# Kernel optimization log

Hardware: AMD Instinct MI355X
Metric: run time of the kernel (lower is better)

Reference implementation:

```python
import jax, jax.numpy as jnp
import numpy as np

WS = 7            # window size
NH = 8            # num heads
C = 128           # hidden size
HS = C // NH      # head size = 16


def _rel_index(ws):
    # Swin-style relative position index for a ws x ws window -> [N, N]
    coords = np.stack(np.meshgrid(np.arange(ws), np.arange(ws), indexing='ij'), 0).reshape(2, -1)
    rel = coords[:, :, None] - coords[:, None, :] + (ws - 1)  # [2, N, N] in [0, 2ws-2]
    return jnp.asarray(rel[0] * (2 * ws - 1) + rel[1])        # [N, N] in [0, (2ws-1)^2)


def setup_inputs() -> dict:
    key = jax.random.key(0)
    ks = jax.random.split(key, 6)
    B, H, W = 16, 112, 112
    s = 0.02
    return {
        'x': jax.random.normal(ks[0], (B, H, W, C), jnp.float32),
        'w_q': jax.random.normal(ks[1], (C, C), jnp.float32) * s,
        'w_k': jax.random.normal(ks[2], (C, C), jnp.float32) * s,
        'w_v': jax.random.normal(ks[3], (C, C), jnp.float32) * s,
        'w_o': jax.random.normal(ks[4], (C, C), jnp.float32) * s,
        'b_o': jnp.zeros((C,), jnp.float32),
        'rel_bias': jax.random.normal(ks[5], ((2 * WS - 1) ** 2, NH), jnp.float32) * s,
    }


def reference(x, w_q, w_k, w_v, w_o, b_o, rel_bias):
    B, H, W, Cc = x.shape
    ws = WS
    N = ws * ws
    # window partition: [B,H,W,C] -> [B*nH*nW, ws*ws, C]
    xw = x.reshape(B, H // ws, ws, W // ws, ws, Cc)
    xw = xw.transpose(0, 1, 3, 2, 4, 5).reshape(-1, N, Cc)
    # qkv projections, split heads: [nW, N, C] -> [nW, NH, N, HS]
    scale = HS ** -0.5
    q = (xw @ w_q).reshape(-1, N, NH, HS).transpose(0, 2, 1, 3) * scale
    k = (xw @ w_k).reshape(-1, N, NH, HS).transpose(0, 2, 1, 3)
    v = (xw @ w_v).reshape(-1, N, NH, HS).transpose(0, 2, 1, 3)
    # attention logits + relative position bias
    attn = jnp.einsum('bhnd,bhmd->bhnm', q, k)
    bias = rel_bias[_rel_index(ws)].transpose(2, 0, 1)  # [NH, N, N]
    attn = jax.nn.softmax(attn + bias[None], axis=-1)
    o = jnp.einsum('bhnm,bhmd->bhnd', attn, v)
    o = o.transpose(0, 2, 1, 3).reshape(-1, N, Cc)
    o = o @ w_o + b_o
    # stitch windows back: [B*nH*nW, N, C] -> [B, H, W, C]
    o = o.reshape(B, H // ws, W // ws, ws, ws, Cc)
    return o.transpose(0, 1, 3, 2, 4, 5).reshape(B, H, W, Cc)
```

## Files before the change

### kernel.cpp

```cpp
#include <hip/hip_runtime.h>

typedef __bf16 bf16_t;
typedef __attribute__((ext_vector_type(8))) __bf16 bf16x8;
typedef __attribute__((ext_vector_type(4))) __bf16 bf16x4;
typedef __attribute__((ext_vector_type(4))) float f32x4;
typedef __attribute__((ext_vector_type(4))) short short4v;

#if __has_builtin(__builtin_amdgcn_mfma_f32_16x16x16bf16_1k)
#define HAVE_MFMA16 1
#else
#define HAVE_MFMA16 0
#endif

#define LDS_XW 0
#define LDS_O  0


__device__ __forceinline__ f32x4 mfma16(bf16x4 a, bf16x4 b, f32x4 c) {
#if HAVE_MFMA16
    return __builtin_amdgcn_mfma_f32_16x16x16bf16_1k(
        __builtin_bit_cast(short4v, a), __builtin_bit_cast(short4v, b), c, 0, 0, 0);
#else
    bf16x8 a8, b8;
#pragma unroll
    for (int j = 0; j < 8; ++j) { a8[j] = (bf16_t)0.0f; b8[j] = (bf16_t)0.0f; }
#pragma unroll
    for (int j = 0; j < 4; ++j) { a8[j] = a[j]; b8[j] = b[j]; }
    return __builtin_amdgcn_mfma_f32_16x16x32_bf16(a8, b8, c, 0, 0, 0);
#endif
}

__global__ void repack_kernel(const float* __restrict__ wq, const float* __restrict__ wk,
                              const float* __restrict__ wv, const float* __restrict__ wo,
                              const float* __restrict__ rel_bias, bf16_t* __restrict__ ws)
{
    int idx = blockIdx.x * 256 + threadIdx.x;
    if (idx < 65536) {
        int mat = idx >> 14;
        int r = idx & 16383;
        int j = r & 7, l = (r >> 3) & 63, nt = (r >> 9) & 7, ks = r >> 12;
        int k = ks * 32 + (l >> 4) * 8 + j;
        int n = nt * 16 + (l & 15);
        const float* w = (mat == 0) ? wq : (mat == 1) ? wk : (mat == 2) ? wv : wo;
        float v = w[k * 128 + n];
        if (mat == 0) v *= 0.25f;
        ws[idx] = (bf16_t)v;
    } else if (idx < 98304) {
        int r = idx - 65536;
        int h = r >> 12, m = (r >> 6) & 63, n = r & 63;
        float v = -10000.0f;
        if (m < 49 && n < 49) {
            int im = m / 7, jm = m % 7, in_ = n / 7, jn = n % 7;
            v = rel_bias[((im - in_ + 6) * 13 + (jm - jn + 6)) * 8 + h];
        }
        ((float*)(ws + 65536))[r] = v;
    }
}

__global__ __launch_bounds__(256, 2)
void win_attn_kernel(const float* __restrict__ x, const float* __restrict__ b_o,
                     const bf16_t* __restrict__ wpack, float* __restrict__ out)
{
    __shared__ __align__(16) unsigned char smem[12544];
    const float* biasT = (const float*)(wpack + 65536);
    const int tid = threadIdx.x;
    const int blk = blockIdx.x;
    const int b  = blk >> 8;
    const int wh = (blk >> 4) & 15;
    const int ww = blk & 15;
    const int wv = tid >> 6;
    const int lane = tid & 63;
    const int c  = lane & 15;
    const int hi = lane >> 4;
    const f32x4 fzero = {0.f, 0.f, 0.f, 0.f};

#pragma unroll
    for (int it = 0; it < 7; ++it) {
        int idx = tid + it * 256;
        if (idx < 1568) {
            int m  = idx >> 5;
            int c4 = idx & 31;
            int i = m / 7, j = m - 7 * i;
            float4 v = *(const float4*)(x + ((b * 112 + wh * 7 + i) * 112 + ww * 7 + j) * 128 + c4 * 4);
            bf16x4 bv;
            bv[0] = (bf16_t)v.x; bv[1] = (bf16_t)v.y; bv[2] = (bf16_t)v.z; bv[3] = (bf16_t)v.w;
            int ch = (c4 >> 1) ^ (m & 7);
            *(bf16x4*)(smem + LDS_XW + m * 256 + ch * 16 + (c4 & 1) * 8) = bv;
        }
    }
    __syncthreads();

    auto xw_frag = [&](int nt, int ks) -> bf16x8 {
        int row = nt * 16 + c;
        int rowc = (row < 49) ? row : 48;
        int ch = (4 * ks + hi) ^ (rowc & 7);
        return *(const bf16x8*)(smem + LDS_XW + rowc * 256 + ch * 16);
    };

    bf16x4 qreg[2][4], kreg[2][4], vreg[4][2];
    {
        bf16x8 wqf[2][4], wkf[2][4];
#pragma unroll
        for (int mt = 0; mt < 2; ++mt)
#pragma unroll
            for (int ks = 0; ks < 4; ++ks) {
                wqf[mt][ks] = *(const bf16x8*)(wpack + 0 * 16384 + ((ks * 8 + (2 * wv + mt)) * 64 + lane) * 8);
                wkf[mt][ks] = *(const bf16x8*)(wpack + 1 * 16384 + ((ks * 8 + (2 * wv + mt)) * 64 + lane) * 8);
            }
#pragma unroll
        for (int nt = 0; nt < 4; ++nt) {
            bf16x8 xf[4];
#pragma unroll
            for (int ks = 0; ks < 4; ++ks) xf[ks] = xw_frag(nt, ks);
            f32x4 aq[2] = {fzero, fzero}, ak[2] = {fzero, fzero};
#pragma unroll
            for (int ks = 0; ks < 4; ++ks)
#pragma unroll
                for (int mt = 0; mt < 2; ++mt) {
                    aq[mt] = __builtin_amdgcn_mfma_f32_16x16x32_bf16(wqf[mt][ks], xf[ks], aq[mt], 0, 0, 0);
                    ak[mt] = __builtin_amdgcn_mfma_f32_16x16x32_bf16(wkf[mt][ks], xf[ks], ak[mt], 0, 0, 0);
                }
#pragma unroll
            for (int mt = 0; mt < 2; ++mt) {
                bf16x4 q, k;
#pragma unroll
                for (int r = 0; r < 4; ++r) { q[r] = (bf16_t)aq[mt][r]; k[r] = (bf16_t)ak[mt][r]; }
                qreg[mt][nt] = q; kreg[mt][nt] = k;
            }
        }
    }
    {
        bf16x8 wvf[2][4];
#pragma unroll
        for (int dt = 0; dt < 2; ++dt)
#pragma unroll
            for (int ks = 0; ks < 4; ++ks)
                wvf[dt][ks] = *(const bf16x8*)(wpack + 2 * 16384 + ((ks * 8 + (2 * wv + dt)) * 64 + lane) * 8);
#pragma unroll
        for (int nt = 0; nt < 4; ++nt) {
            bf16x8 xf[4];
#pragma unroll
            for (int ks = 0; ks < 4; ++ks) xf[ks] = xw_frag(nt, ks);
            f32x4 av[2] = {fzero, fzero};
#pragma unroll
            for (int ks = 0; ks < 4; ++ks)
#pragma unroll
                for (int dt = 0; dt < 2; ++dt)
                    av[dt] = __builtin_amdgcn_mfma_f32_16x16x32_bf16(xf[ks], wvf[dt][ks], av[dt], 0, 0, 0);
#pragma unroll
            for (int dt = 0; dt < 2; ++dt) {
                bf16x4 q;
#pragma unroll
                for (int r = 0; r < 4; ++r) q[r] = (bf16_t)av[dt][r];
                vreg[nt][dt] = q;
            }
        }
    }
    __syncthreads();

#pragma unroll
    for (int hl = 0; hl < 2; ++hl) {
        int h = 2 * wv + hl;
#pragma unroll
        for (int mt = 0; mt < 4; ++mt) {
            int m = mt * 16 + c;
            f32x4 st[4];
#pragma unroll
            for (int nt = 0; nt < 4; ++nt) {
                f32x4 bb = *(const f32x4*)(biasT + (h * 64 + m) * 64 + nt * 16 + 4 * hi);
                st[nt] = mfma16(kreg[hl][nt], qreg[hl][mt], bb);
            }
            float sum = 0.f;
#pragma unroll
            for (int nt = 0; nt < 4; ++nt)
#pragma unroll
                for (int r = 0; r < 4; ++r) {
                    float p = __expf(st[nt][r]);
                    st[nt][r] = p;
                    sum += p;
                }
            sum += __shfl_xor(sum, 16);
            sum += __shfl_xor(sum, 32);
            float inv = 1.f / sum;
            f32x4 oacc = fzero;
#pragma unroll
            for (int nt = 0; nt < 4; ++nt) {
                bf16x4 pv;
#pragma unroll
                for (int r = 0; r < 4; ++r) pv[r] = (bf16_t)(st[nt][r] * inv);
                oacc = mfma16(pv, vreg[nt][hl], oacc);
            }
#pragma unroll
            for (int r = 0; r < 4; ++r) {
                int row = mt * 16 + hi * 4 + r;
                if (row < 49) {
                    int col = 16 * h + c;
                    int ch = (col >> 3) ^ (row & 7);
                    *(bf16_t*)(smem + LDS_O + row * 256 + ch * 16 + (col & 7) * 2) = (bf16_t)oacc[r];
                }
            }
        }
    }
    __syncthreads();

    float bb0 = b_o[32 * wv + c];
    float bb1 = b_o[32 * wv + 16 + c];
#pragma unroll
    for (int mt = 0; mt < 4; ++mt) {
        int row = mt * 16 + c;
        int rowc = (row < 49) ? row : 48;
        f32x4 acc[2] = {fzero, fzero};
#pragma unroll
        for (int ks = 0; ks < 4; ++ks) {
            int ch = (4 * ks + hi) ^ (rowc & 7);
            bf16x8 a = *(const bf16x8*)(smem + LDS_O + rowc * 256 + ch * 16);
            bf16x8 w0 = *(const bf16x8*)(wpack + 3 * 16384 + ((ks * 8 + 2 * wv) * 64 + lane) * 8);
            bf16x8 w1 = *(const bf16x8*)(wpack + 3 * 16384 + ((ks * 8 + 2 * wv + 1) * 64 + lane) * 8);
            acc[0] = __builtin_amdgcn_mfma_f32_16x16x32_bf16(a, w0, acc[0], 0, 0, 0);
            acc[1] = __builtin_amdgcn_mfma_f32_16x16x32_bf16(a, w1, acc[1], 0, 0, 0);
        }
#pragma unroll
        for (int ntl = 0; ntl < 2; ++ntl)
#pragma unroll
            for (int r = 0; r < 4; ++r) {
                int m = mt * 16 + hi * 4 + r;
                if (m < 49) {
                    int i = m / 7, j = m % 7;
                    out[((b * 112 + wh * 7 + i) * 112 + ww * 7 + j) * 128 + 32 * wv + ntl * 16 + c]
                        = acc[ntl][r] + (ntl == 0 ? bb0 : bb1);
                }
            }
    }
}

extern "C" void kernel_launch(void* const* d_in, const int* in_sizes, int n_in,
                              void* d_out, int out_size, void* d_ws, size_t ws_size,
                              hipStream_t stream) {
    const float* x   = (const float*)d_in[0];
    const float* wq  = (const float*)d_in[1];
    const float* wk  = (const float*)d_in[2];
    const float* wvp = (const float*)d_in[3];
    const float* wo  = (const float*)d_in[4];
    const float* bo  = (const float*)d_in[5];
    const float* rb  = (const float*)d_in[6];
    bf16_t* wpack = (bf16_t*)d_ws;

    repack_kernel<<<384, 256, 0, stream>>>(wq, wk, wvp, wo, rb, wpack);
    win_attn_kernel<<<4096, 256, 0, stream>>>(x, bo, wpack, (float*)d_out);
}
```

Before: 119.7 us.

## Restructure QKV projection to cut register pressure and raise occupancy to 3 blocks

Weight fragments are no longer preloaded into large register arrays. They are loaded per k-step inside the projection loops, and Q and K are computed in a non-unrolled loop over the matrix index instead of jointly. V is computed first. Launch bounds are raised from 2 to 3 blocks per CU so more waves can hide latency. In exchange, weight loads are repeated for each row tile, and the runtime-indexed mat loop adds branching and may force spills or dynamic indexing into qreg/kreg.

Measured after the change: 126.7 us. 5.9% more time.

```diff
diff --git a/kernel.cpp b/kernel.cpp
--- a/kernel.cpp
+++ b/kernel.cpp
@@ -57,7 +57,7 @@
     }
 }
 
-__global__ __launch_bounds__(256, 2)
+__global__ __launch_bounds__(256, 3)
 void win_attn_kernel(const float* __restrict__ x, const float* __restrict__ b_o,
                      const bf16_t* __restrict__ wpack, float* __restrict__ out)
 {
@@ -98,61 +98,48 @@
     };
 
     bf16x4 qreg[2][4], kreg[2][4], vreg[4][2];
-    {
-        bf16x8 wqf[2][4], wkf[2][4];
-#pragma unroll
-        for (int mt = 0; mt < 2; ++mt)
-#pragma unroll
-            for (int ks = 0; ks < 4; ++ks) {
-                wqf[mt][ks] = *(const bf16x8*)(wpack + 0 * 16384 + ((ks * 8 + (2 * wv + mt)) * 64 + lane) * 8);
-                wkf[mt][ks] = *(const bf16x8*)(wpack + 1 * 16384 + ((ks * 8 + (2 * wv + mt)) * 64 + lane) * 8);
-            }
+#pragma unroll
+    for (int nt = 0; nt < 4; ++nt) {
+        bf16x8 xf[4];
+#pragma unroll
+        for (int ks = 0; ks < 4; ++ks) xf[ks] = xw_frag(nt, ks);
+        f32x4 av[2] = {fzero, fzero};
+#pragma unroll
+        for (int ks = 0; ks < 4; ++ks) {
+            bf16x8 w0 = *(const bf16x8*)(wpack + 2 * 16384 + ((ks * 8 + 2 * wv) * 64 + lane) * 8);
+            bf16x8 w1 = *(const bf16x8*)(wpack + 2 * 16384 + ((ks * 8 + 2 * wv + 1) * 64 + lane) * 8);
+            av[0] = __builtin_amdgcn_mfma_f32_16x16x32_bf16(xf[ks], w0, av[0], 0, 0, 0);
+            av[1] = __builtin_amdgcn_mfma_f32_16x16x32_bf16(xf[ks], w1, av[1], 0, 0, 0);
+        }
+#pragma unroll
+        for (int dt = 0; dt < 2; ++dt) {
+            bf16x4 q;
+#pragma unroll
+            for (int r = 0; r < 4; ++r) q[r] = (bf16_t)av[dt][r];
+            vreg[nt][dt] = q;
+        }
+    }
+#pragma unroll 1
+    for (int mat = 0; mat < 2; ++mat) {
 #pragma unroll
         for (int nt = 0; nt < 4; ++nt) {
             bf16x8 xf[4];
 #pragma unroll
             for (int ks = 0; ks < 4; ++ks) xf[ks] = xw_frag(nt, ks);
-            f32x4 aq[2] = {fzero, fzero}, ak[2] = {fzero, fzero};
-#pragma unroll
-            for (int ks = 0; ks < 4; ++ks)
-#pragma unroll
-                for (int mt = 0; mt < 2; ++mt) {
-                    aq[mt] = __builtin_amdgcn_mfma_f32_16x16x32_bf16(wqf[mt][ks], xf[ks], aq[mt], 0, 0, 0);
-                    ak[mt] = __builtin_amdgcn_mfma_f32_16x16x32_bf16(wkf[mt][ks], xf[ks], ak[mt], 0, 0, 0);
-                }
-#pragma unroll
-            for (int mt = 0; mt < 2; ++mt) {
-                bf16x4 q, k;
-#pragma unroll
-                for (int r = 0; r < 4; ++r) { q[r] = (bf16_t)aq[mt][r]; k[r] = (bf16_t)ak[mt][r]; }
-                qreg[mt][nt] = q; kreg[mt][nt] = k;
-            }
-        }
-    }
-    {
-        bf16x8 wvf[2][4];
-#pragma unroll
-        for (int dt = 0; dt < 2; ++dt)
-#pragma unroll
-            for (int ks = 0; ks < 4; ++ks)
-                wvf[dt][ks] = *(const bf16x8*)(wpack + 2 * 16384 + ((ks * 8 + (2 * wv + dt)) * 64 + lane) * 8);
-#pragma unroll
-        for (int nt = 0; nt < 4; ++nt) {
-            bf16x8 xf[4];
-#pragma unroll
-            for (int ks = 0; ks < 4; ++ks) xf[ks] = xw_frag(nt, ks);
-            f32x4 av[2] = {fzero, fzero};
-#pragma unroll
-            for (int ks = 0; ks < 4; ++ks)
-#pragma unroll
-                for (int dt = 0; dt < 2; ++dt)
-                    av[dt] = __builtin_amdgcn_mfma_f32_16x16x32_bf16(xf[ks], wvf[dt][ks], av[dt], 0, 0, 0);
-#pragma unroll
-            for (int dt = 0; dt < 2; ++dt) {
+            f32x4 a2[2] = {fzero, fzero};
+#pragma unroll
+            for (int ks = 0; ks < 4; ++ks) {
+                bf16x8 w0 = *(const bf16x8*)(wpack + mat * 16384 + ((ks * 8 + 2 * wv) * 64 + lane) * 8);
+                bf16x8 w1 = *(const bf16x8*)(wpack + mat * 16384 + ((ks * 8 + 2 * wv + 1) * 64 + lane) * 8);
+                a2[0] = __builtin_amdgcn_mfma_f32_16x16x32_bf16(w0, xf[ks], a2[0], 0, 0, 0);
+                a2[1] = __builtin_amdgcn_mfma_f32_16x16x32_bf16(w1, xf[ks], a2[1], 0, 0, 0);
+            }
+#pragma unroll
+            for (int hl = 0; hl < 2; ++hl) {
                 bf16x4 q;
 #pragma unroll
-                for (int r = 0; r < 4; ++r) q[r] = (bf16_t)av[dt][r];
-                vreg[nt][dt] = q;
+                for (int r = 0; r < 4; ++r) q[r] = (bf16_t)a2[hl][r];
+                if (mat == 0) qreg[hl][nt] = q; else kreg[hl][nt] = q;
             }
         }
     }
```
